# Kernel optimization log

Measured on AMD Instinct MI355X. Metric: run time of the kernel, lower is better.

## Reference

```python
import jax, jax.numpy as jnp
import numpy as np

NEG_SLOPE = 0.2  # PyG GATConv leaky_relu slope


def _seg_sum(x, seg, n):
    return jax.ops.segment_sum(x, seg, num_segments=n)


def _seg_softmax(e, seg, n):
    # numerically stable softmax over edges grouped by destination node
    m = jax.ops.segment_max(e, seg, num_segments=n)
    w = jnp.exp(e - m[seg])
    s = jax.ops.segment_sum(w, seg, num_segments=n)
    return w / (s[seg] + 1e-16)


def _gat_bipartite(x_src, x_dst, Ws, Wd, a_s, a_d, b, src, dst, H=4, C=32):
    # PyG GATConv((x_src, x_dst), edge_index), concat=True, add_self_loops=False
    n_dst = x_dst.shape[0]
    hs = (x_src @ Ws).reshape(-1, H, C)   # [Ns,H,C]
    hd = (x_dst @ Wd).reshape(-1, H, C)   # [Nd,H,C]
    es = jnp.einsum('nhc,hc->nh', hs, a_s)  # alpha_src per node
    ed = jnp.einsum('nhc,hc->nh', hd, a_d)  # alpha_dst per node
    e = jax.nn.leaky_relu(es[src] + ed[dst], NEG_SLOPE)  # [E,H]
    alpha = _seg_softmax(e, dst, n_dst)                   # softmax per dst
    out = _seg_sum(hs[src] * alpha[..., None], dst, n_dst)  # [Nd,H,C]
    return out.reshape(n_dst, H * C) + b


def _gcn_self_loops(x, W, b, src, dst):
    # PyG GCNConv with add_self_loops=True, symmetric normalization
    n = x.shape[0]
    xw = x @ W
    deg = _seg_sum(jnp.ones_like(dst, dtype=xw.dtype), dst, n) + 1.0  # +1 self loop
    dinv = jax.lax.rsqrt(deg)
    coef = (dinv[src] * dinv[dst])[:, None]
    agg = _seg_sum(xw[src] * coef, dst, n)
    agg = agg + xw * (dinv * dinv)[:, None]  # self-loop contribution
    return agg + b


def setup_inputs() -> dict:
    D, H, C = 128, 4, 32
    Nb, Nc, Nt = 200_000, 20_000, 2_000
    Eadj, Ebc, Ect = 1_600_000, 200_000, 20_000
    key = jax.random.key(0)
    ks = jax.random.split(key, 24)
    g = 1.0 / np.sqrt(D)
    ga = 1.0 / np.sqrt(C)
    inp = {
        'x_building': jax.random.normal(ks[0], (Nb, D), jnp.float32),
        'x_cable': jax.random.normal(ks[1], (Nc, D), jnp.float32),
        'x_transformer': jax.random.normal(ks[2], (Nt, D), jnp.float32),
        'Ws1': jax.random.normal(ks[3], (D, D), jnp.float32) * g,
        'Wd1': jax.random.normal(ks[4], (D, D), jnp.float32) * g,
        'a_s1': jax.random.normal(ks[5], (H, C), jnp.float32) * ga,
        'a_d1': jax.random.normal(ks[6], (H, C), jnp.float32) * ga,
        'b1': jnp.zeros((D,), jnp.float32),
        'Ws2': jax.random.normal(ks[7], (D, D), jnp.float32) * g,
        'Wd2': jax.random.normal(ks[8], (D, D), jnp.float32) * g,
        'a_s2': jax.random.normal(ks[9], (H, C), jnp.float32) * ga,
        'a_d2': jax.random.normal(ks[10], (H, C), jnp.float32) * ga,
        'b2': jnp.zeros((D,), jnp.float32),
        'Wg': jax.random.normal(ks[11], (D, D), jnp.float32) * g,
        'bg': jnp.zeros((D,), jnp.float32),
        'b2c_src': jax.random.randint(ks[12], (Ebc,), 0, Nb, jnp.int32),
        'b2c_dst': jax.random.randint(ks[13], (Ebc,), 0, Nc, jnp.int32),
        'c2t_src': jax.random.randint(ks[14], (Ect,), 0, Nc, jnp.int32),
        'c2t_dst': jax.random.randint(ks[15], (Ect,), 0, Nt, jnp.int32),
        'adj_src': jax.random.randint(ks[16], (Eadj,), 0, Nb, jnp.int32),
        'adj_dst': jax.random.randint(ks[17], (Eadj,), 0, Nb, jnp.int32),
    }
    return inp


def reference(x_building, x_cable, x_transformer,
              Ws1, Wd1, a_s1, a_d1, b1,
              Ws2, Wd2, a_s2, a_d2, b2,
              Wg, bg,
              b2c_src, b2c_dst, c2t_src, c2t_dst, adj_src, adj_dst):
    # building -> cable_group (GAT), residual 0.5
    h_lv = _gat_bipartite(x_building, x_cable, Ws1, Wd1, a_s1, a_d1, b1,
                          b2c_src, b2c_dst)
    h_cable = x_cable + 0.5 * h_lv
    # (updated) cable_group -> transformer (GAT), residual 0.5
    h_tr = _gat_bipartite(h_cable, x_transformer, Ws2, Wd2, a_s2, a_d2, b2,
                          c2t_src, c2t_dst)
    h_transformer = x_transformer + 0.5 * h_tr
    # building adjacency (GCN with self loops), residual 0.2
    h_adj = _gcn_self_loops(x_building, Wg, bg, adj_src, adj_dst)
    h_building = x_building + 0.2 * h_adj
    return (h_building, h_cable, h_transformer)
```

## Files before the change

kernel.cpp:

```cpp
#include <hip/hip_runtime.h>
#include <hip/hip_bf16.h>
#include <stdint.h>

typedef __attribute__((ext_vector_type(8))) short bf16x8;
typedef __attribute__((ext_vector_type(4))) float floatx4;
typedef __attribute__((ext_vector_type(4))) float f32x4;
typedef __attribute__((ext_vector_type(2))) float f32x2;

__device__ __forceinline__ float2 bf2f(uint32_t u) {
  float2 r;
  r.x = __uint_as_float(u << 16);
  r.y = __uint_as_float(u & 0xffff0000u);
  return r;
}
__device__ __forceinline__ uint16_t f2bf(float f) {
  uint32_t u = __float_as_uint(f);
  uint32_t r = (u + 0x7fffu + ((u >> 16) & 1u)) >> 16;
  return (uint16_t)r;
}
__device__ __forceinline__ uint32_t f2bf_pack(float a, float b) {
  return (uint32_t)f2bf(a) | ((uint32_t)f2bf(b) << 16);
}
__device__ __forceinline__ int iclamp(int v, int lo, int hi) {
  return v < lo ? lo : (v > hi ? hi : v);
}
__device__ __forceinline__ float lrelu(float v) { return v >= 0.f ? v : 0.2f * v; }

__device__ __forceinline__ void acc8(float* a, uint4 r, float w) {
  float2 f0 = bf2f(r.x), f1 = bf2f(r.y), f2 = bf2f(r.z), f3 = bf2f(r.w);
  a[0] += w * f0.x; a[1] += w * f0.y;
  a[2] += w * f1.x; a[3] += w * f1.y;
  a[4] += w * f2.x; a[5] += w * f2.y;
  a[6] += w * f3.x; a[7] += w * f3.y;
}

__global__ void detect_k(const uint32_t* __restrict__ w, int* __restrict__ flag) {
  __shared__ int cnt;
  if (threadIdx.x == 0) cnt = 0;
  __syncthreads();
  uint32_t v = w[threadIdx.x];
  int e = (v >> 23) & 0xFF;
  if (e >= 90 && e <= 160) atomicAdd(&cnt, 1);
  __syncthreads();
  if (threadIdx.x == 0) *flag = (cnt >= 128) ? 1 : 0;
}

__global__ void transp5_k(const void* __restrict__ W0, const void* __restrict__ W1,
                          const void* __restrict__ W2, const void* __restrict__ W3,
                          const void* __restrict__ W4, __hip_bfloat16* __restrict__ WT,
                          const int* __restrict__ flag) {
  int b = blockIdx.x;
  int w = b >> 6;
  int i = (b & 63) * 256 + threadIdx.x;
  const void* W = (w == 0) ? W0 : (w == 1) ? W1 : (w == 2) ? W2 : (w == 3) ? W3 : W4;
  int k = i >> 7, n = i & 127;
  uint16_t h;
  if (*flag)
    h = f2bf(((const float*)W)[i]);
  else
    h = ((const uint16_t*)W)[i];
  ((uint16_t*)WT)[w * 16384 + n * 128 + k] = h;
}

__global__ __launch_bounds__(256) void mm_xw(const void* __restrict__ Abase, size_t aoff,
                                             const __hip_bfloat16* __restrict__ WT,
                                             __hip_bfloat16* __restrict__ out, int M,
                                             const int* __restrict__ flag) {
  __shared__ __align__(16) __hip_bfloat16 w[128 * 136];
  int isf32 = *flag;
  int tid = threadIdx.x;
  for (int i = tid; i < 2048; i += 256) {
    int row = i >> 4, ch = i & 15;
    *(uint4*)&w[row * 136 + ch * 8] = *(const uint4*)&WT[row * 128 + ch * 8];
  }
  __syncthreads();
  int wave = tid >> 6, lane = tid & 63;
  int l15 = lane & 15, kq = (lane >> 4) * 8;
  int row0 = blockIdx.x * 64 + wave * 16;
  int m = row0 + l15;
  int mc = m < M ? m : M - 1;
  floatx4 acc[8];
#pragma unroll
  for (int t = 0; t < 8; t++) acc[t] = (floatx4){0.f, 0.f, 0.f, 0.f};
#pragma unroll
  for (int k0 = 0; k0 < 128; k0 += 32) {
    union { bf16x8 v; uint32_t u[4]; } au;
    size_t eoff = aoff + (size_t)mc * 128 + k0 + kq;
    if (isf32) {
      const f32x4* Af = (const f32x4*)((const float*)Abase + eoff);
      f32x4 f0 = __builtin_nontemporal_load(Af);
      f32x4 f1 = __builtin_nontemporal_load(Af + 1);
      au.u[0] = f2bf_pack(f0.x, f0.y);
      au.u[1] = f2bf_pack(f0.z, f0.w);
      au.u[2] = f2bf_pack(f1.x, f1.y);
      au.u[3] = f2bf_pack(f1.z, f1.w);
    } else {
      au.v = __builtin_nontemporal_load((const bf16x8*)((const __hip_bfloat16*)Abase + eoff));
    }
#pragma unroll
    for (int t = 0; t < 8; t++) {
      bf16x8 b = *(const bf16x8*)&w[(t * 16 + l15) * 136 + k0 + kq];
      acc[t] = __builtin_amdgcn_mfma_f32_16x16x32_bf16(au.v, b, acc[t], 0, 0, 0);
    }
  }
  int rbase = row0 + (lane >> 4) * 4;
  uint16_t* o16 = (uint16_t*)out;
#pragma unroll
  for (int r = 0; r < 4; r++) {
    int rr = rbase + r;
    if (rr < M) {
#pragma unroll
      for (int t = 0; t < 8; t++) o16[(size_t)rr * 128 + t * 16 + l15] = f2bf(acc[t][r]);
    }
  }
}

__global__ void alpha_dot(const __hip_bfloat16* __restrict__ h, const void* __restrict__ a,
                          float* __restrict__ e, int M, const int* __restrict__ flag) {
  int idx = blockIdx.x * 256 + threadIdx.x;
  if (idx >= M * 4) return;
  int isf32 = *flag;
  int m = idx >> 2, hh = idx & 3;
  const uint32_t* hp = (const uint32_t*)(h + (size_t)m * 128 + hh * 32);
  float s = 0.f;
  if (isf32) {
    const float2* ap = (const float2*)((const float*)a + hh * 32);
#pragma unroll
    for (int i = 0; i < 16; i++) {
      float2 hv = bf2f(hp[i]);
      float2 av = ap[i];
      s += hv.x * av.x + hv.y * av.y;
    }
  } else {
    const uint32_t* ap = (const uint32_t*)((const __hip_bfloat16*)a + hh * 32);
#pragma unroll
    for (int i = 0; i < 16; i++) {
      float2 hv = bf2f(hp[i]);
      float2 av = bf2f(ap[i]);
      s += hv.x * av.x + hv.y * av.y;
    }
  }
  e[idx] = s;
}

__global__ void zero2_i32(int* p, int* q, int n) {
  int i = blockIdx.x * 256 + threadIdx.x;
  if (i < n) { p[i] = 0; q[i] = 0; }
}
__global__ void hist_k(const int* __restrict__ dst, int* __restrict__ cnt, int E, int N) {
  int i = blockIdx.x * 256 + threadIdx.x;
  if (i < E) atomicAdd(&cnt[iclamp(dst[i], 0, N - 1)], 1);
}
__global__ void scan_partial(const int* __restrict__ in, int* __restrict__ out,
                             int* __restrict__ bsum, int n) {
  __shared__ int lds[256];
  int t = threadIdx.x;
  int base = blockIdx.x * 1024 + t * 4;
  int v[4];
  int s = 0;
#pragma unroll
  for (int j = 0; j < 4; j++) {
    v[j] = (base + j < n) ? in[base + j] : 0;
    s += v[j];
  }
  lds[t] = s;
  __syncthreads();
  for (int d = 1; d < 256; d <<= 1) {
    int x = 0;
    if (t >= d) x = lds[t - d];
    __syncthreads();
    if (t >= d) lds[t] += x;
    __syncthreads();
  }
  int run = (t > 0) ? lds[t - 1] : 0;
  if (t == 255) bsum[blockIdx.x] = lds[255];
#pragma unroll
  for (int j = 0; j < 4; j++) {
    if (base + j < n) out[base + j] = run;
    run += v[j];
  }
}
__global__ void scan_small2(int* __restrict__ bsum, int nb) {
  __shared__ int lds[256];
  int t = threadIdx.x;
  int v = (t < nb) ? bsum[t] : 0;
  lds[t] = v;
  __syncthreads();
  for (int d = 1; d < 256; d <<= 1) {
    int x = 0;
    if (t >= d) x = lds[t - d];
    __syncthreads();
    if (t >= d) lds[t] += x;
    __syncthreads();
  }
  if (t < nb) bsum[t] = (t > 0) ? lds[t - 1] : 0;
}
__global__ void scan_add(int* out, const int* bsum, const int* __restrict__ cnt,
                         float* __restrict__ dinv, int n) {
  int i = blockIdx.x * 256 + threadIdx.x;
  if (i < n) {
    out[i] += bsum[i >> 10];
    if (dinv) dinv[i] = rsqrtf((float)max(cnt[i], 0) + 1.0f);
  }
}
__global__ void fill_k(const int* __restrict__ src, const int* __restrict__ dst,
                       const int* __restrict__ off, int* __restrict__ cur,
                       int* __restrict__ sorted, int E, int N) {
  int i = blockIdx.x * 256 + threadIdx.x;
  if (i < E) {
    int d = iclamp(dst[i], 0, N - 1);
    int p = off[d] + atomicAdd(&cur[d], 1);
    sorted[iclamp(p, 0, E - 1)] = src[i];
  }
}

__global__ __launch_bounds__(256) void gat_agg(
    const int* __restrict__ off, const int* __restrict__ cnt,
    const int* __restrict__ ssrc, const __hip_bfloat16* __restrict__ hs,
    const float* __restrict__ es, const float* __restrict__ ed,
    const void* __restrict__ xdst, const void* __restrict__ bias,
    void* __restrict__ outb, size_t ooff, int nt_out,
    int N, int Ns, int E, const int* __restrict__ flag) {
  int wid = (blockIdx.x * 256 + threadIdx.x) >> 6;
  if (wid >= N) return;
  int isf32 = *flag;
  int lane = threadIdx.x & 63;
  int g = lane >> 4, il = lane & 15;
  int hh = il >> 2;
  int c8 = il * 8;
  int deg = iclamp(cnt[wid], 0, E);
  int o = iclamp(off[wid], 0, E - deg);
  const int* sp = ssrc + o;
  float edv = ed[wid * 4 + hh];
  float a[8] = {0.f, 0.f, 0.f, 0.f, 0.f, 0.f, 0.f, 0.f};
  float wsum = 0.f;
  for (int e = 0; e < deg; e += 8) {
    int e0 = e + g, e1 = e0 + 4;
    if (e1 < deg) {
      int s0 = iclamp(sp[e0], 0, Ns - 1);
      int s1 = iclamp(sp[e1], 0, Ns - 1);
      uint4 r0 = *(const uint4*)&hs[(size_t)s0 * 128 + c8];
      uint4 r1 = *(const uint4*)&hs[(size_t)s1 * 128 + c8];
      float w0 = __expf(lrelu(es[s0 * 4 + hh] + edv));
      float w1 = __expf(lrelu(es[s1 * 4 + hh] + edv));
      wsum += w0 + w1;
      acc8(a, r0, w0);
      acc8(a, r1, w1);
    } else if (e0 < deg) {
      int s0 = iclamp(sp[e0], 0, Ns - 1);
      uint4 r0 = *(const uint4*)&hs[(size_t)s0 * 128 + c8];
      float w0 = __expf(lrelu(es[s0 * 4 + hh] + edv));
      wsum += w0;
      acc8(a, r0, w0);
    }
  }
#pragma unroll
  for (int j = 0; j < 8; j++) {
    a[j] += __shfl_xor(a[j], 16);
    a[j] += __shfl_xor(a[j], 32);
  }
  wsum += __shfl_xor(wsum, 16);
  wsum += __shfl_xor(wsum, 32);
  float inv = 1.f / (wsum + 1e-16f);
  int cc = c8 + g * 2;
  float v0, v1;
  if (g == 0)      { v0 = a[0]; v1 = a[1]; }
  else if (g == 1) { v0 = a[2]; v1 = a[3]; }
  else if (g == 2) { v0 = a[4]; v1 = a[5]; }
  else             { v0 = a[6]; v1 = a[7]; }
  v0 *= inv; v1 *= inv;
  float x0, x1, b0, b1;
  if (isf32) {
    const float* xf = (const float*)xdst + (size_t)wid * 128 + cc;
    x0 = xf[0]; x1 = xf[1];
    const float* bf_ = (const float*)bias + cc;
    b0 = bf_[0]; b1 = bf_[1];
  } else {
    float2 xf = bf2f(*(const uint32_t*)&((const __hip_bfloat16*)xdst)[(size_t)wid * 128 + cc]);
    float2 bv = bf2f(*(const uint32_t*)&((const __hip_bfloat16*)bias)[cc]);
    x0 = xf.x; x1 = xf.y; b0 = bv.x; b1 = bv.y;
  }
  float r0 = x0 + 0.5f * (v0 + b0);
  float r1 = x1 + 0.5f * (v1 + b1);
  if (isf32) {
    f32x2* op = (f32x2*)((float*)outb + ooff + (size_t)wid * 128 + cc);
    f32x2 rv = {r0, r1};
    if (nt_out) __builtin_nontemporal_store(rv, op);
    else *op = rv;
  } else {
    *(uint32_t*)&((uint16_t*)outb)[ooff + (size_t)wid * 128 + cc] = f2bf_pack(r0, r1);
  }
}

__global__ __launch_bounds__(256) void gcn_agg(
    const int* __restrict__ off, const int* __restrict__ cnt,
    const int* __restrict__ ssrc, const __hip_bfloat16* __restrict__ xw,
    const float* __restrict__ dinv, const void* __restrict__ x,
    const void* __restrict__ bias, void* __restrict__ outb, size_t ooff,
    int N, int E, const int* __restrict__ flag) {
  int wid = (blockIdx.x * 256 + threadIdx.x) >> 6;
  if (wid >= N) return;
  int isf32 = *flag;
  int lane = threadIdx.x & 63;
  int g = lane >> 4, il = lane & 15;
  int c8 = il * 8;
  int deg = iclamp(cnt[wid], 0, E);
  int o = iclamp(off[wid], 0, E - deg);
  const int* sp = ssrc + o;
  float di = dinv[wid];
  float a[8] = {0.f, 0.f, 0.f, 0.f, 0.f, 0.f, 0.f, 0.f};
  for (int e = 0; e < deg; e += 8) {
    int e0 = e + g, e1 = e0 + 4;
    if (e1 < deg) {
      int s0 = iclamp(sp[e0], 0, N - 1);
      int s1 = iclamp(sp[e1], 0, N - 1);
      uint4 r0 = *(const uint4*)&xw[(size_t)s0 * 128 + c8];
      uint4 r1 = *(const uint4*)&xw[(size_t)s1 * 128 + c8];
      float d0 = dinv[s0], d1 = dinv[s1];
      acc8(a, r0, d0);
      acc8(a, r1, d1);
    } else if (e0 < deg) {
      int s0 = iclamp(sp[e0], 0, N - 1);
      uint4 r0 = *(const uint4*)&xw[(size_t)s0 * 128 + c8];
      float d0 = dinv[s0];
      acc8(a, r0, d0);
    }
  }
  if (g == 0) {
    uint4 sr = *(const uint4*)&xw[(size_t)wid * 128 + c8];
    acc8(a, sr, di);
  }
#pragma unroll
  for (int j = 0; j < 8; j++) {
    a[j] += __shfl_xor(a[j], 16);
    a[j] += __shfl_xor(a[j], 32);
  }
  int cc = c8 + g * 2;
  float v0, v1;
  if (g == 0)      { v0 = a[0]; v1 = a[1]; }
  else if (g == 1) { v0 = a[2]; v1 = a[3]; }
  else if (g == 2) { v0 = a[4]; v1 = a[5]; }
  else             { v0 = a[6]; v1 = a[7]; }
  float agg0 = di * v0;
  float agg1 = di * v1;
  float x0, x1, b0, b1;
  if (isf32) {
    f32x2 xf = __builtin_nontemporal_load(
        (const f32x2*)((const float*)x + (size_t)wid * 128 + cc));
    x0 = xf.x; x1 = xf.y;
    const float* bf_ = (const float*)bias + cc;
    b0 = bf_[0]; b1 = bf_[1];
  } else {
    float2 xf = bf2f(*(const uint32_t*)&((const __hip_bfloat16*)x)[(size_t)wid * 128 + cc]);
    float2 bv = bf2f(*(const uint32_t*)&((const __hip_bfloat16*)bias)[cc]);
    x0 = xf.x; x1 = xf.y; b0 = bv.x; b1 = bv.y;
  }
  float r0 = x0 + 0.2f * (agg0 + b0);
  float r1 = x1 + 0.2f * (agg1 + b1);
  if (isf32) {
    f32x2 rv = {r0, r1};
    __builtin_nontemporal_store(rv, (f32x2*)((float*)outb + ooff + (size_t)wid * 128 + cc));
  } else {
    *(uint32_t*)&((uint16_t*)outb)[ooff + (size_t)wid * 128 + cc] = f2bf_pack(r0, r1);
  }
}

extern "C" void kernel_launch(void* const* d_in, const int* in_sizes, int n_in,
                              void* d_out, int out_size, void* d_ws, size_t ws_size,
                              hipStream_t stream) {
  const void* xb = d_in[0];
  const void* xc = d_in[1];
  const void* xt = d_in[2];
  const void* Ws1 = d_in[3];
  const void* Wd1 = d_in[4];
  const void* a_s1 = d_in[5];
  const void* a_d1 = d_in[6];
  const void* b1 = d_in[7];
  const void* Ws2 = d_in[8];
  const void* Wd2 = d_in[9];
  const void* a_s2 = d_in[10];
  const void* a_d2 = d_in[11];
  const void* b2 = d_in[12];
  const void* Wg = d_in[13];
  const void* bg = d_in[14];
  const int* b2c_src = (const int*)d_in[15];
  const int* b2c_dst = (const int*)d_in[16];
  const int* c2t_src = (const int*)d_in[17];
  const int* c2t_dst = (const int*)d_in[18];
  const int* adj_src = (const int*)d_in[19];
  const int* adj_dst = (const int*)d_in[20];

  const int Nb = in_sizes[0] / 128, Nc = in_sizes[1] / 128, Nt = in_sizes[2] / 128;
  const int Ebc = in_sizes[15], Ect = in_sizes[17], Eadj = in_sizes[19];

  auto al = [](size_t x) { return (x + 255) & ~(size_t)255; };
  char* base = (char*)d_ws;

  size_t oFlag = 0;
  size_t oWT = 256;
  size_t oXW = oWT + al(5 * 16384 * 2);
  size_t oPool = oXW + al((size_t)Nb * 256);

  size_t p1 = oPool;
  size_t o_ed1 = p1; p1 += al((size_t)Nc * 16);
  size_t o_hd1 = p1;
  size_t ov = o_hd1;
  size_t o_es1 = ov; ov += al((size_t)Nb * 16);
  size_t o_cntc = ov; ov += al((size_t)Nc * 4);
  size_t o_offc = ov; ov += al((size_t)Nc * 4);
  size_t o_curc = ov; ov += al((size_t)Nc * 4);
  size_t o_srtbc = ov; ov += al((size_t)Ebc * 4);
  size_t o_bs1 = ov; ov += al(1024);
  size_t slot1 = al((size_t)Nc * 256);
  size_t end1 = o_hd1 + (ov - o_hd1 > slot1 ? ov - o_hd1 : slot1);

  size_t p2 = oPool;
  size_t o_hs2 = p2; p2 += al((size_t)Nc * 256);
  size_t o_hd2 = p2; p2 += al((size_t)Nt * 256);
  size_t o_es2 = p2; p2 += al((size_t)Nc * 16);
  size_t o_ed2 = p2; p2 += al((size_t)Nt * 16);
  size_t o_cntt = p2; p2 += al((size_t)Nt * 4);
  size_t o_offt = p2; p2 += al((size_t)Nt * 4);
  size_t o_curt = p2; p2 += al((size_t)Nt * 4);
  size_t o_srtct = p2; p2 += al((size_t)Ect * 4);
  size_t o_bs2 = p2; p2 += al(1024);
  size_t end2 = p2;

  size_t p3 = oPool;
  size_t o_cntb = p3; p3 += al((size_t)Nb * 4);
  size_t o_offb = p3; p3 += al((size_t)Nb * 4);
  size_t o_curb = p3; p3 += al((size_t)Nb * 4);
  size_t o_dinv = p3; p3 += al((size_t)Nb * 4);
  size_t o_srtadj = p3; p3 += al((size_t)Eadj * 4);
  size_t o_bs3 = p3; p3 += al(1024);
  size_t end3 = p3;

  size_t required = end1;
  if (end2 > required) required = end2;
  if (end3 > required) required = end3;
  if (required > ws_size) return;

  int* flag = (int*)(base + oFlag);
  __hip_bfloat16* WT = (__hip_bfloat16*)(base + oWT);
  __hip_bfloat16* XW = (__hip_bfloat16*)(base + oXW);

  const size_t off_b_out = 0;
  const size_t off_c_out = (size_t)Nb * 128;
  const size_t off_t_out = off_c_out + (size_t)Nc * 128;

  detect_k<<<1, 256, 0, stream>>>((const uint32_t*)Ws1, flag);

  transp5_k<<<320, 256, 0, stream>>>(Ws1, Wd1, Ws2, Wd2, Wg, WT, flag);

  {
    __hip_bfloat16* hd1 = (__hip_bfloat16*)(base + o_hd1);
    float* ed1 = (float*)(base + o_ed1);
    mm_xw<<<(Nc + 63) / 64, 256, 0, stream>>>(xc, 0, WT + 1 * 16384, hd1, Nc, flag);
    alpha_dot<<<(Nc * 4 + 255) / 256, 256, 0, stream>>>(hd1, a_d1, ed1, Nc, flag);
    float* es1 = (float*)(base + o_es1);
    int* cnt_c = (int*)(base + o_cntc);
    int* off_c = (int*)(base + o_offc);
    int* cur_c = (int*)(base + o_curc);
    int* srt = (int*)(base + o_srtbc);
    int* bsum = (int*)(base + o_bs1);
    mm_xw<<<(Nb + 63) / 64, 256, 0, stream>>>(xb, 0, WT + 0 * 16384, XW, Nb, flag);
    alpha_dot<<<(Nb * 4 + 255) / 256, 256, 0, stream>>>(XW, a_s1, es1, Nb, flag);
    zero2_i32<<<(Nc + 255) / 256, 256, 0, stream>>>(cnt_c, cur_c, Nc);
    hist_k<<<(Ebc + 255) / 256, 256, 0, stream>>>(b2c_dst, cnt_c, Ebc, Nc);
    int nblk = (Nc + 1023) / 1024;
    scan_partial<<<nblk, 256, 0, stream>>>(cnt_c, off_c, bsum, Nc);
    scan_small2<<<1, 256, 0, stream>>>(bsum, nblk);
    scan_add<<<(Nc + 255) / 256, 256, 0, stream>>>(off_c, bsum, nullptr, nullptr, Nc);
    fill_k<<<(Ebc + 255) / 256, 256, 0, stream>>>(b2c_src, b2c_dst, off_c, cur_c, srt, Ebc, Nc);
    gat_agg<<<(int)(((size_t)Nc * 64 + 255) / 256), 256, 0, stream>>>(
        off_c, cnt_c, srt, XW, es1, ed1, xc, b1, d_out, off_c_out, 0, Nc, Nb, Ebc, flag);
  }

  {
    __hip_bfloat16* hs2 = (__hip_bfloat16*)(base + o_hs2);
    __hip_bfloat16* hd2 = (__hip_bfloat16*)(base + o_hd2);
    float* es2 = (float*)(base + o_es2);
    float* ed2 = (float*)(base + o_ed2);
    int* cnt_t = (int*)(base + o_cntt);
    int* off_t = (int*)(base + o_offt);
    int* cur_t = (int*)(base + o_curt);
    int* srt = (int*)(base + o_srtct);
    int* bsum = (int*)(base + o_bs2);
    mm_xw<<<(Nc + 63) / 64, 256, 0, stream>>>(d_out, off_c_out, WT + 2 * 16384, hs2, Nc, flag);
    mm_xw<<<(Nt + 63) / 64, 256, 0, stream>>>(xt, 0, WT + 3 * 16384, hd2, Nt, flag);
    alpha_dot<<<(Nc * 4 + 255) / 256, 256, 0, stream>>>(hs2, a_s2, es2, Nc, flag);
    alpha_dot<<<(Nt * 4 + 255) / 256, 256, 0, stream>>>(hd2, a_d2, ed2, Nt, flag);
    zero2_i32<<<(Nt + 255) / 256, 256, 0, stream>>>(cnt_t, cur_t, Nt);
    hist_k<<<(Ect + 255) / 256, 256, 0, stream>>>(c2t_dst, cnt_t, Ect, Nt);
    int nblk = (Nt + 1023) / 1024;
    scan_partial<<<nblk, 256, 0, stream>>>(cnt_t, off_t, bsum, Nt);
    scan_small2<<<1, 256, 0, stream>>>(bsum, nblk);
    scan_add<<<(Nt + 255) / 256, 256, 0, stream>>>(off_t, bsum, nullptr, nullptr, Nt);
    fill_k<<<(Ect + 255) / 256, 256, 0, stream>>>(c2t_src, c2t_dst, off_t, cur_t, srt, Ect, Nt);
    gat_agg<<<(int)(((size_t)Nt * 64 + 255) / 256), 256, 0, stream>>>(
        off_t, cnt_t, srt, hs2, es2, ed2, xt, b2, d_out, off_t_out, 1, Nt, Nc, Ect, flag);
  }

  {
    int* cnt_b = (int*)(base + o_cntb);
    int* off_b = (int*)(base + o_offb);
    int* cur_b = (int*)(base + o_curb);
    float* dinv = (float*)(base + o_dinv);
    int* srt = (int*)(base + o_srtadj);
    int* bsum = (int*)(base + o_bs3);
    mm_xw<<<(Nb + 63) / 64, 256, 0, stream>>>(xb, 0, WT + 4 * 16384, XW, Nb, flag);
    zero2_i32<<<(Nb + 255) / 256, 256, 0, stream>>>(cnt_b, cur_b, Nb);
    hist_k<<<(Eadj + 255) / 256, 256, 0, stream>>>(adj_dst, cnt_b, Eadj, Nb);
    int nblk = (Nb + 1023) / 1024;
    scan_partial<<<nblk, 256, 0, stream>>>(cnt_b, off_b, bsum, Nb);
    scan_small2<<<1, 256, 0, stream>>>(bsum, nblk);
    scan_add<<<(Nb + 255) / 256, 256, 0, stream>>>(off_b, bsum, cnt_b, dinv, Nb);
    fill_k<<<(Eadj + 255) / 256, 256, 0, stream>>>(adj_src, adj_dst, off_b, cur_b, srt, Eadj, Nb);
    gcn_agg<<<(int)(((size_t)Nb * 64 + 255) / 256), 256, 0, stream>>>(
        off_b, cnt_b, srt, XW, dinv, xb, bg, d_out, off_b_out, Nb, Eadj, flag);
  }
}
```

Baseline: 701.1 us.

## Batch graph preprocessing and matmuls across all three convolutions, fuse alpha dot

Merges the per-graph zero/histogram/scan/fill kernels into single launches that cover all three edge sets. The three input-side matmuls and then the two second-stage matmuls are grouped into batched kernels. The attention dot products are computed inside the matmul epilogue through shuffles instead of separate alpha_dot passes. The detection kernel is folded into each kernel as a wave ballot. This cuts launch count, re-reading of the XW buffer, and serialization between small kernels. The cost is a larger workspace, since buffers are no longer aliased, and a per-kernel dtype detection.

```diff
diff --git a/kernel.cpp b/kernel.cpp
--- a/kernel.cpp
+++ b/kernel.cpp
@@ -25,6 +25,13 @@
   return v < lo ? lo : (v > hi ? hi : v);
 }
 __device__ __forceinline__ float lrelu(float v) { return v >= 0.f ? v : 0.2f * v; }
+
+__device__ __forceinline__ int detect_f32(const uint32_t* __restrict__ det) {
+  uint32_t v = det[threadIdx.x & 63];
+  int e = (v >> 23) & 0xFF;
+  unsigned long long b = __ballot(e >= 90 && e <= 160);
+  return __popcll(b) >= 48;
+}
 
 __device__ __forceinline__ void acc8(float* a, uint4 r, float w) {
   float2 f0 = bf2f(r.x), f1 = bf2f(r.y), f2 = bf2f(r.z), f3 = bf2f(r.w);
@@ -34,49 +41,172 @@
   a[6] += w * f3.x; a[7] += w * f3.y;
 }
 
-__global__ void detect_k(const uint32_t* __restrict__ w, int* __restrict__ flag) {
-  __shared__ int cnt;
-  if (threadIdx.x == 0) cnt = 0;
-  __syncthreads();
-  uint32_t v = w[threadIdx.x];
-  int e = (v >> 23) & 0xFF;
-  if (e >= 90 && e <= 160) atomicAdd(&cnt, 1);
-  __syncthreads();
-  if (threadIdx.x == 0) *flag = (cnt >= 128) ? 1 : 0;
-}
-
-__global__ void transp5_k(const void* __restrict__ W0, const void* __restrict__ W1,
-                          const void* __restrict__ W2, const void* __restrict__ W3,
-                          const void* __restrict__ W4, __hip_bfloat16* __restrict__ WT,
-                          const int* __restrict__ flag) {
+__global__ void transp_zero(const void* __restrict__ W0, const void* __restrict__ W1,
+                            const void* __restrict__ W2, const void* __restrict__ W3,
+                            const void* __restrict__ W4, __hip_bfloat16* __restrict__ WT,
+                            int* __restrict__ zp, int zn, const uint32_t* __restrict__ det) {
+  int isf32 = detect_f32(det);
   int b = blockIdx.x;
   int w = b >> 6;
   int i = (b & 63) * 256 + threadIdx.x;
   const void* W = (w == 0) ? W0 : (w == 1) ? W1 : (w == 2) ? W2 : (w == 3) ? W3 : W4;
   int k = i >> 7, n = i & 127;
   uint16_t h;
-  if (*flag)
+  if (isf32)
     h = f2bf(((const float*)W)[i]);
   else
     h = ((const uint16_t*)W)[i];
   ((uint16_t*)WT)[w * 16384 + n * 128 + k] = h;
-}
-
-__global__ __launch_bounds__(256) void mm_xw(const void* __restrict__ Abase, size_t aoff,
-                                             const __hip_bfloat16* __restrict__ WT,
-                                             __hip_bfloat16* __restrict__ out, int M,
-                                             const int* __restrict__ flag) {
+  for (int j = blockIdx.x * 256 + threadIdx.x; j < zn; j += gridDim.x * 256) zp[j] = 0;
+}
+
+__global__ void hist_all(const int* __restrict__ d0, int E0, const int* __restrict__ d1,
+                         int E1, const int* __restrict__ d2, int E2,
+                         int* __restrict__ cnt, int n0, int n1, int n2) {
+  int i = blockIdx.x * 256 + threadIdx.x;
+  if (i < E0) {
+    atomicAdd(&cnt[iclamp(d0[i], 0, n0 - 1)], 1);
+  } else if (i < E0 + E1) {
+    int j = i - E0;
+    atomicAdd(&cnt[n0 + iclamp(d1[j], 0, n1 - 1)], 1);
+  } else if (i < E0 + E1 + E2) {
+    int j = i - E0 - E1;
+    atomicAdd(&cnt[n0 + n1 + iclamp(d2[j], 0, n2 - 1)], 1);
+  }
+}
+
+__global__ void scanp_all(const int* __restrict__ cnt, int* __restrict__ off,
+                          int* __restrict__ bsum, int n0, int n1, int n2,
+                          int nb0, int nb1) {
+  int b = blockIdx.x;
+  int seg, lb, base, n;
+  if (b < nb0) { seg = 0; lb = b; base = 0; n = n0; }
+  else if (b < nb0 + nb1) { seg = 1; lb = b - nb0; base = n0; n = n1; }
+  else { seg = 2; lb = b - nb0 - nb1; base = n0 + n1; n = n2; }
+  const int* in = cnt + base;
+  int* out = off + base;
+  int* bs = bsum + seg * 256;
+  __shared__ int lds[256];
+  int t = threadIdx.x;
+  int pbase = lb * 1024 + t * 4;
+  int v[4];
+  int s = 0;
+#pragma unroll
+  for (int j = 0; j < 4; j++) {
+    v[j] = (pbase + j < n) ? in[pbase + j] : 0;
+    s += v[j];
+  }
+  lds[t] = s;
+  __syncthreads();
+  for (int d = 1; d < 256; d <<= 1) {
+    int x = 0;
+    if (t >= d) x = lds[t - d];
+    __syncthreads();
+    if (t >= d) lds[t] += x;
+    __syncthreads();
+  }
+  int run = (t > 0) ? lds[t - 1] : 0;
+  if (t == 255) bs[lb] = lds[255];
+#pragma unroll
+  for (int j = 0; j < 4; j++) {
+    if (pbase + j < n) out[pbase + j] = run;
+    run += v[j];
+  }
+}
+
+__global__ void scans_all(int* __restrict__ bsum, int nb0, int nb1, int nb2) {
+  int seg = blockIdx.x;
+  int nb = (seg == 0) ? nb0 : (seg == 1) ? nb1 : nb2;
+  int* bs = bsum + seg * 256;
+  __shared__ int lds[256];
+  int t = threadIdx.x;
+  int v = (t < nb) ? bs[t] : 0;
+  lds[t] = v;
+  __syncthreads();
+  for (int d = 1; d < 256; d <<= 1) {
+    int x = 0;
+    if (t >= d) x = lds[t - d];
+    __syncthreads();
+    if (t >= d) lds[t] += x;
+    __syncthreads();
+  }
+  if (t < nb) bs[t] = (t > 0) ? lds[t - 1] : 0;
+}
+
+__global__ void scanadd_dinv(int* __restrict__ off, const int* __restrict__ bsum,
+                             const int* __restrict__ cnt, float* __restrict__ dinv,
+                             int n0, int n1, int n2) {
+  int i = blockIdx.x * 256 + threadIdx.x;
+  if (i >= n0 + n1 + n2) return;
+  int seg, li;
+  if (i < n0) { seg = 0; li = i; }
+  else if (i < n0 + n1) { seg = 1; li = i - n0; }
+  else { seg = 2; li = i - n0 - n1; }
+  off[i] += bsum[seg * 256 + (li >> 10)];
+  if (seg == 2) dinv[li] = rsqrtf((float)max(cnt[i], 0) + 1.0f);
+}
+
+__global__ void fill_all(const int* __restrict__ s0, const int* __restrict__ d0, int E0,
+                         const int* __restrict__ s1, const int* __restrict__ d1, int E1,
+                         const int* __restrict__ s2, const int* __restrict__ d2, int E2,
+                         const int* __restrict__ off, int* __restrict__ cur,
+                         int* __restrict__ r0, int* __restrict__ r1, int* __restrict__ r2,
+                         int n0, int n1, int n2) {
+  int i = blockIdx.x * 256 + threadIdx.x;
+  const int* sp;
+  const int* dp;
+  int* rp;
+  int base, N, E, j;
+  if (i < E0) { sp = s0; dp = d0; rp = r0; base = 0; N = n0; E = E0; j = i; }
+  else if (i < E0 + E1) { sp = s1; dp = d1; rp = r1; base = n0; N = n1; E = E1; j = i - E0; }
+  else if (i < E0 + E1 + E2) { sp = s2; dp = d2; rp = r2; base = n0 + n1; N = n2; E = E2; j = i - E0 - E1; }
+  else return;
+  int d = iclamp(dp[j], 0, N - 1);
+  int gi = base + d;
+  int p = off[gi] + atomicAdd(&cur[gi], 1);
+  rp[iclamp(p, 0, E - 1)] = sp[j];
+}
+
+struct MMB {
+  const void* A0; const void* A1; const void* A2;
+  unsigned long long ao0, ao1, ao2;
+  const __hip_bfloat16* W0; const __hip_bfloat16* W1; const __hip_bfloat16* W2;
+  __hip_bfloat16* O0; __hip_bfloat16* O1; __hip_bfloat16* O2;
+  float* E0; float* E1; float* E2;
+  const void* V0; const void* V1; const void* V2;
+  int M0, M1, M2, B1, B2;
+};
+
+__global__ __launch_bounds__(256) void mm_batch(MMB p, const uint32_t* __restrict__ det) {
+  int isf32 = detect_f32(det);
+  const void* Abase;
+  size_t aoff;
+  const __hip_bfloat16* WTp;
+  __hip_bfloat16* out;
+  float* esp;
+  const void* av;
+  int M, bRow;
+  int bid = (int)blockIdx.x;
+  if (bid >= p.B2) {
+    Abase = p.A2; aoff = p.ao2; WTp = p.W2; out = p.O2; esp = p.E2; av = p.V2;
+    M = p.M2; bRow = bid - p.B2;
+  } else if (bid >= p.B1) {
+    Abase = p.A1; aoff = p.ao1; WTp = p.W1; out = p.O1; esp = p.E1; av = p.V1;
+    M = p.M1; bRow = bid - p.B1;
+  } else {
+    Abase = p.A0; aoff = p.ao0; WTp = p.W0; out = p.O0; esp = p.E0; av = p.V0;
+    M = p.M0; bRow = bid;
+  }
   __shared__ __align__(16) __hip_bfloat16 w[128 * 136];
-  int isf32 = *flag;
   int tid = threadIdx.x;
   for (int i = tid; i < 2048; i += 256) {
     int row = i >> 4, ch = i & 15;
-    *(uint4*)&w[row * 136 + ch * 8] = *(const uint4*)&WT[row * 128 + ch * 8];
+    *(uint4*)&w[row * 136 + ch * 8] = *(const uint4*)&WTp[row * 128 + ch * 8];
   }
   __syncthreads();
   int wave = tid >> 6, lane = tid & 63;
   int l15 = lane & 15, kq = (lane >> 4) * 8;
-  int row0 = blockIdx.x * 64 + wave * 16;
+  int row0 = bRow * 64 + wave * 16;
   int m = row0 + l15;
   int mc = m < M ? m : M - 1;
   floatx4 acc[8];
@@ -113,104 +243,42 @@
       for (int t = 0; t < 8; t++) o16[(size_t)rr * 128 + t * 16 + l15] = f2bf(acc[t][r]);
     }
   }
-}
-
-__global__ void alpha_dot(const __hip_bfloat16* __restrict__ h, const void* __restrict__ a,
-                          float* __restrict__ e, int M, const int* __restrict__ flag) {
-  int idx = blockIdx.x * 256 + threadIdx.x;
-  if (idx >= M * 4) return;
-  int isf32 = *flag;
-  int m = idx >> 2, hh = idx & 3;
-  const uint32_t* hp = (const uint32_t*)(h + (size_t)m * 128 + hh * 32);
-  float s = 0.f;
-  if (isf32) {
-    const float2* ap = (const float2*)((const float*)a + hh * 32);
-#pragma unroll
-    for (int i = 0; i < 16; i++) {
-      float2 hv = bf2f(hp[i]);
-      float2 av = ap[i];
-      s += hv.x * av.x + hv.y * av.y;
+  if (esp) {
+    float av8[8];
+    if (isf32) {
+      const float* af = (const float*)av;
+#pragma unroll
+      for (int t = 0; t < 8; t++) av8[t] = af[t * 16 + l15];
+    } else {
+      const uint16_t* ab = (const uint16_t*)av;
+#pragma unroll
+      for (int t = 0; t < 8; t++) av8[t] = __uint_as_float((uint32_t)ab[t * 16 + l15] << 16);
     }
-  } else {
-    const uint32_t* ap = (const uint32_t*)((const __hip_bfloat16*)a + hh * 32);
-#pragma unroll
-    for (int i = 0; i < 16; i++) {
-      float2 hv = bf2f(hp[i]);
-      float2 av = bf2f(ap[i]);
-      s += hv.x * av.x + hv.y * av.y;
-    }
-  }
-  e[idx] = s;
-}
-
-__global__ void zero2_i32(int* p, int* q, int n) {
-  int i = blockIdx.x * 256 + threadIdx.x;
-  if (i < n) { p[i] = 0; q[i] = 0; }
-}
-__global__ void hist_k(const int* __restrict__ dst, int* __restrict__ cnt, int E, int N) {
-  int i = blockIdx.x * 256 + threadIdx.x;
-  if (i < E) atomicAdd(&cnt[iclamp(dst[i], 0, N - 1)], 1);
-}
-__global__ void scan_partial(const int* __restrict__ in, int* __restrict__ out,
-                             int* __restrict__ bsum, int n) {
-  __shared__ int lds[256];
-  int t = threadIdx.x;
-  int base = blockIdx.x * 1024 + t * 4;
-  int v[4];
-  int s = 0;
-#pragma unroll
-  for (int j = 0; j < 4; j++) {
-    v[j] = (base + j < n) ? in[base + j] : 0;
-    s += v[j];
-  }
-  lds[t] = s;
-  __syncthreads();
-  for (int d = 1; d < 256; d <<= 1) {
-    int x = 0;
-    if (t >= d) x = lds[t - d];
-    __syncthreads();
-    if (t >= d) lds[t] += x;
-    __syncthreads();
-  }
-  int run = (t > 0) ? lds[t - 1] : 0;
-  if (t == 255) bsum[blockIdx.x] = lds[255];
-#pragma unroll
-  for (int j = 0; j < 4; j++) {
-    if (base + j < n) out[base + j] = run;
-    run += v[j];
-  }
-}
-__global__ void scan_small2(int* __restrict__ bsum, int nb) {
-  __shared__ int lds[256];
-  int t = threadIdx.x;
-  int v = (t < nb) ? bsum[t] : 0;
-  lds[t] = v;
-  __syncthreads();
-  for (int d = 1; d < 256; d <<= 1) {
-    int x = 0;
-    if (t >= d) x = lds[t - d];
-    __syncthreads();
-    if (t >= d) lds[t] += x;
-    __syncthreads();
-  }
-  if (t < nb) bsum[t] = (t > 0) ? lds[t - 1] : 0;
-}
-__global__ void scan_add(int* out, const int* bsum, const int* __restrict__ cnt,
-                         float* __restrict__ dinv, int n) {
-  int i = blockIdx.x * 256 + threadIdx.x;
-  if (i < n) {
-    out[i] += bsum[i >> 10];
-    if (dinv) dinv[i] = rsqrtf((float)max(cnt[i], 0) + 1.0f);
-  }
-}
-__global__ void fill_k(const int* __restrict__ src, const int* __restrict__ dst,
-                       const int* __restrict__ off, int* __restrict__ cur,
-                       int* __restrict__ sorted, int E, int N) {
-  int i = blockIdx.x * 256 + threadIdx.x;
-  if (i < E) {
-    int d = iclamp(dst[i], 0, N - 1);
-    int p = off[d] + atomicAdd(&cur[d], 1);
-    sorted[iclamp(p, 0, E - 1)] = src[i];
+    float ph[4][4];
+#pragma unroll
+    for (int h = 0; h < 4; h++)
+#pragma unroll
+      for (int r = 0; r < 4; r++)
+        ph[h][r] = acc[2 * h][r] * av8[2 * h] + acc[2 * h + 1][r] * av8[2 * h + 1];
+#pragma unroll
+    for (int h = 0; h < 4; h++)
+#pragma unroll
+      for (int r = 0; r < 4; r++) {
+        float v = ph[h][r];
+        v += __shfl_xor(v, 1);
+        v += __shfl_xor(v, 2);
+        v += __shfl_xor(v, 4);
+        v += __shfl_xor(v, 8);
+        ph[h][r] = v;
+      }
+    int rr = l15 >> 2, hh = l15 & 3;
+    float s0 = (hh == 0) ? ph[0][0] : (hh == 1) ? ph[1][0] : (hh == 2) ? ph[2][0] : ph[3][0];
+    float s1 = (hh == 0) ? ph[0][1] : (hh == 1) ? ph[1][1] : (hh == 2) ? ph[2][1] : ph[3][1];
+    float s2 = (hh == 0) ? ph[0][2] : (hh == 1) ? ph[1][2] : (hh == 2) ? ph[2][2] : ph[3][2];
+    float s3 = (hh == 0) ? ph[0][3] : (hh == 1) ? ph[1][3] : (hh == 2) ? ph[2][3] : ph[3][3];
+    float val = (rr == 0) ? s0 : (rr == 1) ? s1 : (rr == 2) ? s2 : s3;
+    int rowA = row0 + (lane >> 4) * 4 + rr;
+    if (rowA < M) esp[(size_t)rowA * 4 + hh] = val;
   }
 }
 
@@ -220,10 +288,10 @@
     const float* __restrict__ es, const float* __restrict__ ed,
     const void* __restrict__ xdst, const void* __restrict__ bias,
     void* __restrict__ outb, size_t ooff, int nt_out,
-    int N, int Ns, int E, const int* __restrict__ flag) {
+    int N, int Ns, int E, const uint32_t* __restrict__ det) {
+  int isf32 = detect_f32(det);
   int wid = (blockIdx.x * 256 + threadIdx.x) >> 6;
   if (wid >= N) return;
-  int isf32 = *flag;
   int lane = threadIdx.x & 63;
   int g = lane >> 4, il = lane & 15;
   int hh = il >> 2;
@@ -297,10 +365,10 @@
     const int* __restrict__ ssrc, const __hip_bfloat16* __restrict__ xw,
     const float* __restrict__ dinv, const void* __restrict__ x,
     const void* __restrict__ bias, void* __restrict__ outb, size_t ooff,
-    int N, int E, const int* __restrict__ flag) {
+    int N, int E, const uint32_t* __restrict__ det) {
+  int isf32 = detect_f32(det);
   int wid = (blockIdx.x * 256 + threadIdx.x) >> 6;
   if (wid >= N) return;
-  int isf32 = *flag;
   int lane = threadIdx.x & 63;
   int g = lane >> 4, il = lane & 15;
   int c8 = il * 8;
@@ -392,131 +460,105 @@
 
   const int Nb = in_sizes[0] / 128, Nc = in_sizes[1] / 128, Nt = in_sizes[2] / 128;
   const int Ebc = in_sizes[15], Ect = in_sizes[17], Eadj = in_sizes[19];
+  const int nAll = Nc + Nt + Nb;
+  const int Eall = Ebc + Ect + Eadj;
 
   auto al = [](size_t x) { return (x + 255) & ~(size_t)255; };
   char* base = (char*)d_ws;
 
-  size_t oFlag = 0;
-  size_t oWT = 256;
-  size_t oXW = oWT + al(5 * 16384 * 2);
-  size_t oPool = oXW + al((size_t)Nb * 256);
-
-  size_t p1 = oPool;
-  size_t o_ed1 = p1; p1 += al((size_t)Nc * 16);
-  size_t o_hd1 = p1;
-  size_t ov = o_hd1;
-  size_t o_es1 = ov; ov += al((size_t)Nb * 16);
-  size_t o_cntc = ov; ov += al((size_t)Nc * 4);
-  size_t o_offc = ov; ov += al((size_t)Nc * 4);
-  size_t o_curc = ov; ov += al((size_t)Nc * 4);
-  size_t o_srtbc = ov; ov += al((size_t)Ebc * 4);
-  size_t o_bs1 = ov; ov += al(1024);
-  size_t slot1 = al((size_t)Nc * 256);
-  size_t end1 = o_hd1 + (ov - o_hd1 > slot1 ? ov - o_hd1 : slot1);
-
-  size_t p2 = oPool;
-  size_t o_hs2 = p2; p2 += al((size_t)Nc * 256);
-  size_t o_hd2 = p2; p2 += al((size_t)Nt * 256);
-  size_t o_es2 = p2; p2 += al((size_t)Nc * 16);
-  size_t o_ed2 = p2; p2 += al((size_t)Nt * 16);
-  size_t o_cntt = p2; p2 += al((size_t)Nt * 4);
-  size_t o_offt = p2; p2 += al((size_t)Nt * 4);
-  size_t o_curt = p2; p2 += al((size_t)Nt * 4);
-  size_t o_srtct = p2; p2 += al((size_t)Ect * 4);
-  size_t o_bs2 = p2; p2 += al(1024);
-  size_t end2 = p2;
-
-  size_t p3 = oPool;
-  size_t o_cntb = p3; p3 += al((size_t)Nb * 4);
-  size_t o_offb = p3; p3 += al((size_t)Nb * 4);
-  size_t o_curb = p3; p3 += al((size_t)Nb * 4);
-  size_t o_dinv = p3; p3 += al((size_t)Nb * 4);
-  size_t o_srtadj = p3; p3 += al((size_t)Eadj * 4);
-  size_t o_bs3 = p3; p3 += al(1024);
-  size_t end3 = p3;
-
-  size_t required = end1;
-  if (end2 > required) required = end2;
-  if (end3 > required) required = end3;
-  if (required > ws_size) return;
-
-  int* flag = (int*)(base + oFlag);
-  __hip_bfloat16* WT = (__hip_bfloat16*)(base + oWT);
-  __hip_bfloat16* XW = (__hip_bfloat16*)(base + oXW);
+  size_t o = 0;
+  size_t o_WT = o;    o += al((size_t)5 * 16384 * 2);
+  size_t o_cnt = o;   o += al((size_t)nAll * 4);
+  size_t o_cur = o;   o += al((size_t)nAll * 4);
+  size_t o_off = o;   o += al((size_t)nAll * 4);
+  size_t o_dinv = o;  o += al((size_t)Nb * 4);
+  size_t o_bsum = o;  o += al(3 * 256 * 4);
+  size_t o_srtbc = o; o += al((size_t)Ebc * 4);
+  size_t o_srtct = o; o += al((size_t)Ect * 4);
+  size_t o_srtadj = o; o += al((size_t)Eadj * 4);
+  size_t o_es1 = o;   o += al((size_t)Nb * 16);
+  size_t o_ed1 = o;   o += al((size_t)Nc * 16);
+  size_t o_es2 = o;   o += al((size_t)Nc * 16);
+  size_t o_ed2 = o;   o += al((size_t)Nt * 16);
+  size_t o_hd1 = o;   o += al((size_t)Nc * 256);
+  size_t o_hd2 = o;   o += al((size_t)Nt * 256);
+  size_t o_hs2 = o;   o += al((size_t)Nc * 256);
+  size_t o_XW = o;    o += al((size_t)Nb * 256);
+  if (o > ws_size) return;
+
+  const uint32_t* det = (const uint32_t*)Ws1;
+  __hip_bfloat16* WT = (__hip_bfloat16*)(base + o_WT);
+  int* cnt = (int*)(base + o_cnt);
+  int* cur = (int*)(base + o_cur);
+  int* off = (int*)(base + o_off);
+  float* dinv = (float*)(base + o_dinv);
+  int* bsum = (int*)(base + o_bsum);
+  int* srt_bc = (int*)(base + o_srtbc);
+  int* srt_ct = (int*)(base + o_srtct);
+  int* srt_adj = (int*)(base + o_srtadj);
+  float* es1 = (float*)(base + o_es1);
+  float* ed1 = (float*)(base + o_ed1);
+  float* es2 = (float*)(base + o_es2);
+  float* ed2 = (float*)(base + o_ed2);
+  __hip_bfloat16* hd1 = (__hip_bfloat16*)(base + o_hd1);
+  __hip_bfloat16* hd2 = (__hip_bfloat16*)(base + o_hd2);
+  __hip_bfloat16* hs2 = (__hip_bfloat16*)(base + o_hs2);
+  __hip_bfloat16* XW = (__hip_bfloat16*)(base + o_XW);
 
   const size_t off_b_out = 0;
   const size_t off_c_out = (size_t)Nb * 128;
   const size_t off_t_out = off_c_out + (size_t)Nc * 128;
 
-  detect_k<<<1, 256, 0, stream>>>((const uint32_t*)Ws1, flag);
-
-  transp5_k<<<320, 256, 0, stream>>>(Ws1, Wd1, Ws2, Wd2, Wg, WT, flag);
+  int* cnt_c = cnt;
+  int* cnt_t = cnt + Nc;
+  int* cnt_b = cnt + Nc + Nt;
+  int* off_c = off;
+  int* off_t = off + Nc;
+  int* off_b = off + Nc + Nt;
+
+  int zn = (int)((o_off - o_cnt) / 4);
+  transp_zero<<<320, 256, 0, stream>>>(Ws1, Wd1, Ws2, Wd2, Wg, WT, cnt, zn, det);
+
+  hist_all<<<(Eall + 255) / 256, 256, 0, stream>>>(b2c_dst, Ebc, c2t_dst, Ect, adj_dst,
+                                                   Eadj, cnt, Nc, Nt, Nb);
+
+  int nb0 = (Nc + 1023) / 1024, nb1 = (Nt + 1023) / 1024, nb2 = (Nb + 1023) / 1024;
+  scanp_all<<<nb0 + nb1 + nb2, 256, 0, stream>>>(cnt, off, bsum, Nc, Nt, Nb, nb0, nb1);
+  scans_all<<<3, 256, 0, stream>>>(bsum, nb0, nb1, nb2);
+  scanadd_dinv<<<(nAll + 255) / 256, 256, 0, stream>>>(off, bsum, cnt, dinv, Nc, Nt, Nb);
+
+  fill_all<<<(Eall + 255) / 256, 256, 0, stream>>>(b2c_src, b2c_dst, Ebc, c2t_src, c2t_dst,
+                                                   Ect, adj_src, adj_dst, Eadj, off, cur,
+                                                   srt_bc, srt_ct, srt_adj, Nc, Nt, Nb);
 
   {
-    __hip_bfloat16* hd1 = (__hip_bfloat16*)(base + o_hd1);
-    float* ed1 = (float*)(base + o_ed1);
-    mm_xw<<<(Nc + 63) / 64, 256, 0, stream>>>(xc, 0, WT + 1 * 16384, hd1, Nc, flag);
-    alpha_dot<<<(Nc * 4 + 255) / 256, 256, 0, stream>>>(hd1, a_d1, ed1, Nc, flag);
-    float* es1 = (float*)(base + o_es1);
-    int* cnt_c = (int*)(base + o_cntc);
-    int* off_c = (int*)(base + o_offc);
-    int* cur_c = (int*)(base + o_curc);
-    int* srt = (int*)(base + o_srtbc);
-    int* bsum = (int*)(base + o_bs1);
-    mm_xw<<<(Nb + 63) / 64, 256, 0, stream>>>(xb, 0, WT + 0 * 16384, XW, Nb, flag);
-    alpha_dot<<<(Nb * 4 + 255) / 256, 256, 0, stream>>>(XW, a_s1, es1, Nb, flag);
-    zero2_i32<<<(Nc + 255) / 256, 256, 0, stream>>>(cnt_c, cur_c, Nc);
-    hist_k<<<(Ebc + 255) / 256, 256, 0, stream>>>(b2c_dst, cnt_c, Ebc, Nc);
-    int nblk = (Nc + 1023) / 1024;
-    scan_partial<<<nblk, 256, 0, stream>>>(cnt_c, off_c, bsum, Nc);
-    scan_small2<<<1, 256, 0, stream>>>(bsum, nblk);
-    scan_add<<<(Nc + 255) / 256, 256, 0, stream>>>(off_c, bsum, nullptr, nullptr, Nc);
-    fill_k<<<(Ebc + 255) / 256, 256, 0, stream>>>(b2c_src, b2c_dst, off_c, cur_c, srt, Ebc, Nc);
-    gat_agg<<<(int)(((size_t)Nc * 64 + 255) / 256), 256, 0, stream>>>(
-        off_c, cnt_c, srt, XW, es1, ed1, xc, b1, d_out, off_c_out, 0, Nc, Nb, Ebc, flag);
-  }
+    MMB p;
+    p.A0 = xb; p.ao0 = 0; p.W0 = WT + 0 * 16384; p.O0 = XW; p.E0 = es1; p.V0 = a_s1; p.M0 = Nb;
+    p.A1 = xc; p.ao1 = 0; p.W1 = WT + 1 * 16384; p.O1 = hd1; p.E1 = ed1; p.V1 = a_d1; p.M1 = Nc;
+    p.A2 = xt; p.ao2 = 0; p.W2 = WT + 3 * 16384; p.O2 = hd2; p.E2 = ed2; p.V2 = a_d2; p.M2 = Nt;
+    int g0 = (Nb + 63) / 64, g1 = (Nc + 63) / 64, g2 = (Nt + 63) / 64;
+    p.B1 = g0; p.B2 = g0 + g1;
+    mm_batch<<<g0 + g1 + g2, 256, 0, stream>>>(p, det);
+  }
+
+  gat_agg<<<(int)(((size_t)Nc * 64 + 255) / 256), 256, 0, stream>>>(
+      off_c, cnt_c, srt_bc, XW, es1, ed1, xc, b1, d_out, off_c_out, 0, Nc, Nb, Ebc, det);
 
   {
-    __hip_bfloat16* hs2 = (__hip_bfloat16*)(base + o_hs2);
-    __hip_bfloat16* hd2 = (__hip_bfloat16*)(base + o_hd2);
-    float* es2 = (float*)(base + o_es2);
-    float* ed2 = (float*)(base + o_ed2);
-    int* cnt_t = (int*)(base + o_cntt);
-    int* off_t = (int*)(base + o_offt);
-    int* cur_t = (int*)(base + o_curt);
-    int* srt = (int*)(base + o_srtct);
-    int* bsum = (int*)(base + o_bs2);
-    mm_xw<<<(Nc + 63) / 64, 256, 0, stream>>>(d_out, off_c_out, WT + 2 * 16384, hs2, Nc, flag);
-    mm_xw<<<(Nt + 63) / 64, 256, 0, stream>>>(xt, 0, WT + 3 * 16384, hd2, Nt, flag);
-    alpha_dot<<<(Nc * 4 + 255) / 256, 256, 0, stream>>>(hs2, a_s2, es2, Nc, flag);
-    alpha_dot<<<(Nt * 4 + 255) / 256, 256, 0, stream>>>(hd2, a_d2, ed2, Nt, flag);
-    zero2_i32<<<(Nt + 255) / 256, 256, 0, stream>>>(cnt_t, cur_t, Nt);
-    hist_k<<<(Ect + 255) / 256, 256, 0, stream>>>(c2t_dst, cnt_t, Ect, Nt);
-    int nblk = (Nt + 1023) / 1024;
-    scan_partial<<<nblk, 256, 0, stream>>>(cnt_t, off_t, bsum, Nt);
-    scan_small2<<<1, 256, 0, stream>>>(bsum, nblk);
-    scan_add<<<(Nt + 255) / 256, 256, 0, stream>>>(off_t, bsum, nullptr, nullptr, Nt);
-    fill_k<<<(Ect + 255) / 256, 256, 0, stream>>>(c2t_src, c2t_dst, off_t, cur_t, srt, Ect, Nt);
-    gat_agg<<<(int)(((size_t)Nt * 64 + 255) / 256), 256, 0, stream>>>(
-        off_t, cnt_t, srt, hs2, es2, ed2, xt, b2, d_out, off_t_out, 1, Nt, Nc, Ect, flag);
-  }
-
-  {
-    int* cnt_b = (int*)(base + o_cntb);
-    int* off_b = (int*)(base + o_offb);
-    int* cur_b = (int*)(base + o_curb);
-    float* dinv = (float*)(base + o_dinv);
-    int* srt = (int*)(base + o_srtadj);
-    int* bsum = (int*)(base + o_bs3);
-    mm_xw<<<(Nb + 63) / 64, 256, 0, stream>>>(xb, 0, WT + 4 * 16384, XW, Nb, flag);
-    zero2_i32<<<(Nb + 255) / 256, 256, 0, stream>>>(cnt_b, cur_b, Nb);
-    hist_k<<<(Eadj + 255) / 256, 256, 0, stream>>>(adj_dst, cnt_b, Eadj, Nb);
-    int nblk = (Nb + 1023) / 1024;
-    scan_partial<<<nblk, 256, 0, stream>>>(cnt_b, off_b, bsum, Nb);
-    scan_small2<<<1, 256, 0, stream>>>(bsum, nblk);
-    scan_add<<<(Nb + 255) / 256, 256, 0, stream>>>(off_b, bsum, cnt_b, dinv, Nb);
-    fill_k<<<(Eadj + 255) / 256, 256, 0, stream>>>(adj_src, adj_dst, off_b, cur_b, srt, Eadj, Nb);
-    gcn_agg<<<(int)(((size_t)Nb * 64 + 255) / 256), 256, 0, stream>>>(
-        off_b, cnt_b, srt, XW, dinv, xb, bg, d_out, off_b_out, Nb, Eadj, flag);
-  }
-}
+    MMB p;
+    p.A0 = d_out; p.ao0 = off_c_out; p.W0 = WT + 2 * 16384; p.O0 = hs2; p.E0 = es2;
+    p.V0 = a_s2; p.M0 = Nc;
+    p.A1 = xb; p.ao1 = 0; p.W1 = WT + 4 * 16384; p.O1 = XW; p.E1 = nullptr;
+    p.V1 = nullptr; p.M1 = Nb;
+    p.A2 = xb; p.ao2 = 0; p.W2 = WT; p.O2 = XW; p.E2 = nullptr; p.V2 = nullptr; p.M2 = 0;
+    int g0 = (Nc + 63) / 64, g1 = (Nb + 63) / 64;
+    p.B1 = g0; p.B2 = g0 + g1;
+    mm_batch<<<g0 + g1, 256, 0, stream>>>(p, det);
+  }
+
+  gat_agg<<<(int)(((size_t)Nt * 64 + 255) / 256), 256, 0, stream>>>(
+      off_t, cnt_t, srt_ct, hs2, es2, ed2, xt, b2, d_out, off_t_out, 1, Nt, Nc, Ect, det);
+
+  gcn_agg<<<(int)(((size_t)Nb * 64 + 255) / 256), 256, 0, stream>>>(
+      off_b, cnt_b, srt_adj, XW, dinv, xb, bg, d_out, off_b_out, Nb, Eadj, det);
+}
```

Measured after the change: 628.9 us. -10.3%, faster.
